# Optimization experiments

Measured on AMD Instinct MI355X. Metric: run time of the kernel, lower is better.

## Reference

```python
import jax, jax.numpy as jnp
import numpy as np
import math

D_K = 64
DROP_P = 0.5

def setup_inputs() -> dict:
    key = jax.random.key(0)
    kq, kk, kv, km = jax.random.split(key, 4)
    B, S, d = 32, 2048, D_K
    Q = jax.random.normal(kq, (B, S, d), dtype=jnp.float32)
    K = jax.random.normal(kk, (B, S, d), dtype=jnp.float32)
    V = jax.random.normal(kv, (B, S, d), dtype=jnp.float32)
    # Bernoulli(keep_prob) mask for training-mode dropout (p=0.5)
    dropout_mask = jax.random.bernoulli(km, 1.0 - DROP_P, (B, S, S))
    return {"Q": Q, "K": K, "V": V, "dropout_mask": dropout_mask}

def reference(Q, K, V, dropout_mask):
    # attn = softmax(Q K^T / sqrt(d_k)); dropout; y = attn V
    scale = 1.0 / math.sqrt(D_K)
    scores = jnp.einsum('bqd,bkd->bqk', Q, K) * scale   # [B,S,S]
    attn = jax.nn.softmax(scores, axis=-1)
    keep_scale = 1.0 / (1.0 - DROP_P)
    attn = jnp.where(dropout_mask, attn * keep_scale, 0.0)
    y = jnp.einsum('bqk,bkd->bqd', attn, V)             # [B,S,d]
    return (y, attn)
```

## Files before the change

### kernel.cpp

```cpp
#include <hip/hip_runtime.h>
#include <hip/hip_bf16.h>
#include <stdint.h>

#define SQ 2048
#define DK 64
#define NB 32
#define TQ 16
#define EW 2064
#define SCL 0.18033688011112042f

typedef __attribute__((ext_vector_type(8))) short short8;
typedef __attribute__((ext_vector_type(4))) float f32x4;
typedef __attribute__((ext_vector_type(4))) unsigned u32x4;
typedef __attribute__((ext_vector_type(2))) unsigned u32x2;

__device__ __forceinline__ unsigned f2bf_u(float x) {
    unsigned u = __builtin_bit_cast(unsigned, x);
    u += 0x7fffu + ((u >> 16) & 1u);
    return u >> 16;
}
__device__ __forceinline__ float bf2f(unsigned h) {
    return __builtin_bit_cast(float, h << 16);
}
__device__ __forceinline__ float bf2f_hi(unsigned u) {
    return __builtin_bit_cast(float, u & 0xffff0000u);
}
__device__ __forceinline__ unsigned cvtpk_bf16(float lo, float hi) {
    unsigned r;
    asm("v_cvt_pk_bf16_f32 %0, %1, %2" : "=v"(r) : "v"(lo), "v"(hi));
    return r;
}
__device__ __forceinline__ void split8(const float* p, short8& h, short8& l) {
    f32x4 a = *(const f32x4*)p;
    f32x4 b = *(const f32x4*)(p + 4);
    #pragma unroll
    for (int j = 0; j < 4; ++j) {
        unsigned ua = f2bf_u(a[j]);
        h[j] = (short)ua; l[j] = (short)f2bf_u(a[j] - bf2f(ua));
        unsigned ub = f2bf_u(b[j]);
        h[j + 4] = (short)ub; l[j + 4] = (short)f2bf_u(b[j] - bf2f(ub));
    }
}

__global__ __launch_bounds__(256) void prep_kernel(
    const float* __restrict__ K, const float* __restrict__ V,
    const unsigned* __restrict__ Mk,
    unsigned short* __restrict__ Khi, unsigned short* __restrict__ Klo,
    unsigned short* __restrict__ Vt, unsigned* __restrict__ Mkb)
{
    __shared__ float vtile[64][65];
    const int t = threadIdx.x;

    if (blockIdx.x >= NB * 32) {
        const size_t w = (size_t)(blockIdx.x - NB * 32) * 256 + t;
        const unsigned* p = Mk + w * 32;
        unsigned bits = 0;
        #pragma unroll
        for (int j = 0; j < 8; ++j) {
            const u32x4 v = *(const u32x4*)(p + j * 4);
            bits |= (v[0] ? 1u : 0u) << (j * 4 + 0);
            bits |= (v[1] ? 1u : 0u) << (j * 4 + 1);
            bits |= (v[2] ? 1u : 0u) << (j * 4 + 2);
            bits |= (v[3] ? 1u : 0u) << (j * 4 + 3);
        }
        Mkb[w] = bits;
        return;
    }

    const int b  = blockIdx.x >> 5;
    const int s0 = (blockIdx.x & 31) << 6;
    const size_t base = ((size_t)b * SQ + s0) * DK + (size_t)t * 16;

    {
        short8 h0, l0, h1, l1;
        split8(K + base,     h0, l0);
        split8(K + base + 8, h1, l1);
        *(short8*)(Khi + base)     = h0;
        *(short8*)(Khi + base + 8) = h1;
        *(short8*)(Klo + base)     = l0;
        *(short8*)(Klo + base + 8) = l1;
    }
    {
        const int sr = t >> 2, dc = (t & 3) << 4;
        #pragma unroll
        for (int u = 0; u < 16; u += 4) {
            f32x4 v = *(const f32x4*)(V + base + u);
            vtile[sr][dc + u + 0] = v[0];
            vtile[sr][dc + u + 1] = v[1];
            vtile[sr][dc + u + 2] = v[2];
            vtile[sr][dc + u + 3] = v[3];
        }
    }
    __syncthreads();
    #pragma unroll
    for (int rep = 0; rep < 16; ++rep) {
        const int idx = rep * 256 + t;
        const int d = idx >> 6, s = idx & 63;
        Vt[((size_t)b * DK + d) * SQ + s0 + s] = (unsigned short)f2bf_u(vtile[s][d]);
    }
}

__global__ __launch_bounds__(512, 4) void sdpa_main(
    const float* __restrict__ Q, const unsigned short* __restrict__ Khi,
    const unsigned short* __restrict__ Klo, const unsigned short* __restrict__ Vt,
    const unsigned* __restrict__ Mkb, float* __restrict__ Yout, float* __restrict__ Aout)
{
    __shared__ __align__(16) unsigned short e_lds[TQ][EW];
    __shared__ float yp[4][TQ][16];
    __shared__ float rsum[8][TQ];
    __shared__ float i2s[TQ];

    const int tid  = threadIdx.x;
    const int lane = tid & 63;
    const int wv   = tid >> 6;
    const int m16  = lane & 15;
    const int kq   = lane >> 4;
    const int koff = kq * 8;

    const int bx  = blockIdx.x;
    const int xcd = bx & 7;
    const int j   = bx >> 3;
    const int b   = xcd * 4 + (j >> 7);
    const int q0  = (j & 127) * TQ;

    short8 qh[2], ql[2];
    {
        const float* qrow = Q + ((size_t)b * SQ + q0 + m16) * DK;
        split8(qrow + koff,      qh[0], ql[0]);
        split8(qrow + 32 + koff, qh[1], ql[1]);
    }

    const unsigned* mrow = Mkb + ((size_t)b * SQ + q0 + m16) * (SQ / 32) + wv * 8;
    const u32x4 mA = *(const u32x4*)mrow;
    const u32x4 mB = *(const u32x4*)(mrow + 4);

    float rs = 0.f;
    {
        const size_t krow = ((size_t)b * SQ + wv * 256 + m16) * DK;
        const unsigned short* khp = Khi + krow;
        const unsigned short* klp = Klo + krow;
        const int xw = (m16 & 7) << 3;
        #pragma unroll
        for (int t = 0; t < 16; ++t) {
            const int off = t * 16 * DK;
            const short8 kh0 = *(const short8*)(khp + off + koff);
            const short8 kh1 = *(const short8*)(khp + off + 32 + koff);
            const short8 kl0 = *(const short8*)(klp + off + koff);
            const short8 kl1 = *(const short8*)(klp + off + 32 + koff);
            f32x4 a0 = {0.f, 0.f, 0.f, 0.f};
            f32x4 a1 = {0.f, 0.f, 0.f, 0.f};
            a0 = __builtin_amdgcn_mfma_f32_16x16x32_bf16(kh0, qh[0], a0, 0, 0, 0);
            a1 = __builtin_amdgcn_mfma_f32_16x16x32_bf16(kh1, qh[1], a1, 0, 0, 0);
            a0 = __builtin_amdgcn_mfma_f32_16x16x32_bf16(kh0, ql[0], a0, 0, 0, 0);
            a1 = __builtin_amdgcn_mfma_f32_16x16x32_bf16(kh1, ql[1], a1, 0, 0, 0);
            a0 = __builtin_amdgcn_mfma_f32_16x16x32_bf16(kl0, qh[0], a0, 0, 0, 0);
            a1 = __builtin_amdgcn_mfma_f32_16x16x32_bf16(kl1, qh[1], a1, 0, 0, 0);
            const float e0 = __builtin_amdgcn_exp2f((a0[0] + a1[0]) * SCL);
            const float e1 = __builtin_amdgcn_exp2f((a0[1] + a1[1]) * SCL);
            const float e2 = __builtin_amdgcn_exp2f((a0[2] + a1[2]) * SCL);
            const float e3 = __builtin_amdgcn_exp2f((a0[3] + a1[3]) * SCL);
            rs += (e0 + e1) + (e2 + e3);
            const unsigned mword = (t < 8) ? mA[t >> 1] : mB[(t >> 1) - 4];
            const unsigned bits = mword >> ((t & 1) * 16 + kq * 4);
            const float p0 = (bits & 1u) ? e0 : 0.f;
            const float p1 = (bits & 2u) ? e1 : 0.f;
            const float p2 = (bits & 4u) ? e2 : 0.f;
            const float p3 = (bits & 8u) ? e3 : 0.f;
            u32x2 pk;
            pk[0] = cvtpk_bf16(p0, p1);
            pk[1] = cvtpk_bf16(p2, p3);
            *(u32x2*)&e_lds[m16][(wv * 256 + t * 16 + kq * 4) ^ xw] = pk;
        }
    }
    rs += __shfl_xor(rs, 16);
    rs += __shfl_xor(rs, 32);
    if (lane < 16) rsum[wv][lane] = rs;
    __syncthreads();
    if (tid < 16) {
        float s = 0.f;
        #pragma unroll
        for (int w = 0; w < 8; ++w) s += rsum[w][tid];
        i2s[tid] = 2.0f / s;
    }
    __syncthreads();

    const int cr = tid >> 5;
    const int cc = (tid & 31) * 8;
    const int xc = (cr & 7) << 3;
    const float i2 = i2s[cr];
    const size_t crow = ((size_t)b * SQ + q0 + cr) * SQ + cc;

    const int g    = wv >> 1;
    const int par  = wv & 1;
    const int xm   = (m16 & 7) << 3;
    const unsigned short* vrow = Vt + ((size_t)b * DK + g * 16 + m16) * SQ;
    f32x4 acc = {0.f, 0.f, 0.f, 0.f};

    #define CSTRIPE(s)                                                            \
    {                                                                             \
        const u32x4 ev = *(const u32x4*)&e_lds[cr][((s) * 256 + cc) ^ xc];        \
        f32x4 o0, o1;                                                             \
        o0[0] = bf2f(ev[0] & 0xffffu) * i2;  o0[1] = bf2f_hi(ev[0]) * i2;         \
        o0[2] = bf2f(ev[1] & 0xffffu) * i2;  o0[3] = bf2f_hi(ev[1]) * i2;         \
        o1[0] = bf2f(ev[2] & 0xffffu) * i2;  o1[1] = bf2f_hi(ev[2]) * i2;         \
        o1[2] = bf2f(ev[3] & 0xffffu) * i2;  o1[3] = bf2f_hi(ev[3]) * i2;         \
        __builtin_nontemporal_store(o0, (f32x4*)(Aout + crow + (s) * 256));       \
        __builtin_nontemporal_store(o1, (f32x4*)(Aout + crow + (s) * 256 + 4));   \
    }
    #define PVCHUNK4(c0)                                                          \
    {                                                                             \
        _Pragma("unroll")                                                         \
        for (int c = (c0); c < (c0) + 4; ++c) {                                   \
            const int kl = par * 1024 + c * 32;                                   \
            const short8 af = *(const short8*)&e_lds[m16][(kl + koff) ^ xm];      \
            const short8 vf = *(const short8*)(vrow + kl + koff);                 \
            acc = __builtin_amdgcn_mfma_f32_16x16x32_bf16(af, vf, acc, 0, 0, 0);  \
        }                                                                         \
    }

    CSTRIPE(0) PVCHUNK4(0)
    CSTRIPE(1) PVCHUNK4(4)
    CSTRIPE(2) PVCHUNK4(8)
    CSTRIPE(3) PVCHUNK4(12)
    CSTRIPE(4) PVCHUNK4(16)
    CSTRIPE(5) PVCHUNK4(20)
    CSTRIPE(6) PVCHUNK4(24)
    CSTRIPE(7) PVCHUNK4(28)

    #undef PVCHUNK4
    #undef CSTRIPE

    if (par == 1) {
        #pragma unroll
        for (int r = 0; r < 4; ++r) yp[g][kq * 4 + r][m16] = acc[r];
    }
    __syncthreads();
    if (par == 0) {
        #pragma unroll
        for (int r = 0; r < 4; ++r) {
            const float yv = (acc[r] + yp[g][kq * 4 + r][m16]) * i2s[kq * 4 + r];
            Yout[((size_t)b * SQ + q0 + kq * 4 + r) * DK + g * 16 + m16] = yv;
        }
    }
}

extern "C" void kernel_launch(void* const* d_in, const int* in_sizes, int n_in,
                              void* d_out, int out_size, void* d_ws, size_t ws_size,
                              hipStream_t stream) {
    const float*    Q  = (const float*)d_in[0];
    const float*    K  = (const float*)d_in[1];
    const float*    V  = (const float*)d_in[2];
    const unsigned* Mk = (const unsigned*)d_in[3];
    float* Yout = (float*)d_out;
    float* Aout = (float*)d_out + (size_t)NB * SQ * DK;

    const size_t NEL = (size_t)NB * SQ * DK;
    unsigned short* Khi = (unsigned short*)d_ws;
    unsigned short* Klo = Khi + NEL;
    unsigned short* Vt  = Klo + NEL;
    unsigned*       Mkb = (unsigned*)(Vt + NEL);

    const int NPREP = NB * 32;
    const int NMKP  = (int)((size_t)NB * SQ * (SQ / 32) / 256);
    prep_kernel<<<dim3(NPREP + NMKP), dim3(256), 0, stream>>>(K, V, Mk, Khi, Klo, Vt, Mkb);
    sdpa_main<<<dim3(NB * (SQ / TQ)), dim3(512), 0, stream>>>(
        Q, Khi, Klo, Vt, Mkb, Yout, Aout);
}
```

Baseline: 530.7 us.

## Split key dimension across two blocks with redundant row-sum and partial-Y reduction

Each query tile is now handled by two blocks, each owning half of the key range. Every block still computes the full QK^T row sums so normalisation stays exact, but only the owning waves write bf16 probabilities to shared memory. Each block then does half of the attention output stores and half of the PV product, writing partial Y to a workspace that a new kernel sums. Shared memory per block is halved and launch bounds are raised to allow more resident blocks. The cost is doubled QK^T matmul and exp work, an extra kernel launch, and extra global traffic for partial Y.

```diff
diff --git a/kernel.cpp b/kernel.cpp
--- a/kernel.cpp
+++ b/kernel.cpp
@@ -6,7 +6,8 @@
 #define DK 64
 #define NB 32
 #define TQ 16
-#define EW 2064
+#define KH 1024
+#define EW 1032
 #define SCL 0.18033688011112042f
 
 typedef __attribute__((ext_vector_type(8))) short short8;
@@ -100,12 +101,12 @@
     }
 }
 
-__global__ __launch_bounds__(512, 4) void sdpa_main(
+__global__ __launch_bounds__(512, 8) void sdpa_main(
     const float* __restrict__ Q, const unsigned short* __restrict__ Khi,
     const unsigned short* __restrict__ Klo, const unsigned short* __restrict__ Vt,
-    const unsigned* __restrict__ Mkb, float* __restrict__ Yout, float* __restrict__ Aout)
+    const unsigned* __restrict__ Mkb, float* __restrict__ Yp, float* __restrict__ Aout)
 {
-    __shared__ __align__(16) unsigned short e_lds[TQ][EW];
+    __shared__ __align__(16) unsigned short e_half[TQ][EW];
     __shared__ float yp[4][TQ][16];
     __shared__ float rsum[8][TQ];
     __shared__ float i2s[TQ];
@@ -117,11 +118,16 @@
     const int kq   = lane >> 4;
     const int koff = kq * 8;
 
-    const int bx  = blockIdx.x;
-    const int xcd = bx & 7;
-    const int j   = bx >> 3;
-    const int b   = xcd * 4 + (j >> 7);
-    const int q0  = (j & 127) * TQ;
+    const int bx   = blockIdx.x;
+    const int xcd  = bx & 7;
+    const int j    = bx >> 3;
+    const int b    = xcd * 4 + (j >> 8);
+    const int rest = j & 255;
+    const int q0   = (rest >> 1) * TQ;
+    const int kh   = rest & 1;
+
+    const int wlocal = wv & 3;
+    const bool owned = (wv >> 2) == kh;
 
     short8 qh[2], ql[2];
     {
@@ -129,10 +135,6 @@
         split8(qrow + koff,      qh[0], ql[0]);
         split8(qrow + 32 + koff, qh[1], ql[1]);
     }
-
-    const unsigned* mrow = Mkb + ((size_t)b * SQ + q0 + m16) * (SQ / 32) + wv * 8;
-    const u32x4 mA = *(const u32x4*)mrow;
-    const u32x4 mB = *(const u32x4*)(mrow + 4);
 
     float rs = 0.f;
     {
@@ -140,36 +142,63 @@
         const unsigned short* khp = Khi + krow;
         const unsigned short* klp = Klo + krow;
         const int xw = (m16 & 7) << 3;
-        #pragma unroll
-        for (int t = 0; t < 16; ++t) {
-            const int off = t * 16 * DK;
-            const short8 kh0 = *(const short8*)(khp + off + koff);
-            const short8 kh1 = *(const short8*)(khp + off + 32 + koff);
-            const short8 kl0 = *(const short8*)(klp + off + koff);
-            const short8 kl1 = *(const short8*)(klp + off + 32 + koff);
-            f32x4 a0 = {0.f, 0.f, 0.f, 0.f};
-            f32x4 a1 = {0.f, 0.f, 0.f, 0.f};
-            a0 = __builtin_amdgcn_mfma_f32_16x16x32_bf16(kh0, qh[0], a0, 0, 0, 0);
-            a1 = __builtin_amdgcn_mfma_f32_16x16x32_bf16(kh1, qh[1], a1, 0, 0, 0);
-            a0 = __builtin_amdgcn_mfma_f32_16x16x32_bf16(kh0, ql[0], a0, 0, 0, 0);
-            a1 = __builtin_amdgcn_mfma_f32_16x16x32_bf16(kh1, ql[1], a1, 0, 0, 0);
-            a0 = __builtin_amdgcn_mfma_f32_16x16x32_bf16(kl0, qh[0], a0, 0, 0, 0);
-            a1 = __builtin_amdgcn_mfma_f32_16x16x32_bf16(kl1, qh[1], a1, 0, 0, 0);
-            const float e0 = __builtin_amdgcn_exp2f((a0[0] + a1[0]) * SCL);
-            const float e1 = __builtin_amdgcn_exp2f((a0[1] + a1[1]) * SCL);
-            const float e2 = __builtin_amdgcn_exp2f((a0[2] + a1[2]) * SCL);
-            const float e3 = __builtin_amdgcn_exp2f((a0[3] + a1[3]) * SCL);
-            rs += (e0 + e1) + (e2 + e3);
-            const unsigned mword = (t < 8) ? mA[t >> 1] : mB[(t >> 1) - 4];
-            const unsigned bits = mword >> ((t & 1) * 16 + kq * 4);
-            const float p0 = (bits & 1u) ? e0 : 0.f;
-            const float p1 = (bits & 2u) ? e1 : 0.f;
-            const float p2 = (bits & 4u) ? e2 : 0.f;
-            const float p3 = (bits & 8u) ? e3 : 0.f;
-            u32x2 pk;
-            pk[0] = cvtpk_bf16(p0, p1);
-            pk[1] = cvtpk_bf16(p2, p3);
-            *(u32x2*)&e_lds[m16][(wv * 256 + t * 16 + kq * 4) ^ xw] = pk;
+
+        if (owned) {
+            const unsigned* mrow = Mkb + ((size_t)b * SQ + q0 + m16) * (SQ / 32) + wv * 8;
+            const u32x4 mA = *(const u32x4*)mrow;
+            const u32x4 mB = *(const u32x4*)(mrow + 4);
+            #pragma unroll
+            for (int t = 0; t < 16; ++t) {
+                const int off = t * 16 * DK;
+                const short8 kh0 = *(const short8*)(khp + off + koff);
+                const short8 kh1 = *(const short8*)(khp + off + 32 + koff);
+                const short8 kl0 = *(const short8*)(klp + off + koff);
+                const short8 kl1 = *(const short8*)(klp + off + 32 + koff);
+                f32x4 a0 = {0.f, 0.f, 0.f, 0.f};
+                f32x4 a1 = {0.f, 0.f, 0.f, 0.f};
+                a0 = __builtin_amdgcn_mfma_f32_16x16x32_bf16(kh0, qh[0], a0, 0, 0, 0);
+                a1 = __builtin_amdgcn_mfma_f32_16x16x32_bf16(kh1, qh[1], a1, 0, 0, 0);
+                a0 = __builtin_amdgcn_mfma_f32_16x16x32_bf16(kh0, ql[0], a0, 0, 0, 0);
+                a1 = __builtin_amdgcn_mfma_f32_16x16x32_bf16(kh1, ql[1], a1, 0, 0, 0);
+                a0 = __builtin_amdgcn_mfma_f32_16x16x32_bf16(kl0, qh[0], a0, 0, 0, 0);
+                a1 = __builtin_amdgcn_mfma_f32_16x16x32_bf16(kl1, qh[1], a1, 0, 0, 0);
+                const float e0 = __builtin_amdgcn_exp2f((a0[0] + a1[0]) * SCL);
+                const float e1 = __builtin_amdgcn_exp2f((a0[1] + a1[1]) * SCL);
+                const float e2 = __builtin_amdgcn_exp2f((a0[2] + a1[2]) * SCL);
+                const float e3 = __builtin_amdgcn_exp2f((a0[3] + a1[3]) * SCL);
+                rs += (e0 + e1) + (e2 + e3);
+                const unsigned mword = (t < 8) ? mA[t >> 1] : mB[(t >> 1) - 4];
+                const unsigned bits = mword >> ((t & 1) * 16 + kq * 4);
+                const float p0 = (bits & 1u) ? e0 : 0.f;
+                const float p1 = (bits & 2u) ? e1 : 0.f;
+                const float p2 = (bits & 4u) ? e2 : 0.f;
+                const float p3 = (bits & 8u) ? e3 : 0.f;
+                u32x2 pk;
+                pk[0] = cvtpk_bf16(p0, p1);
+                pk[1] = cvtpk_bf16(p2, p3);
+                *(u32x2*)&e_half[m16][(wlocal * 256 + t * 16 + kq * 4) ^ xw] = pk;
+            }
+        } else {
+            #pragma unroll
+            for (int t = 0; t < 16; ++t) {
+                const int off = t * 16 * DK;
+                const short8 kh0 = *(const short8*)(khp + off + koff);
+                const short8 kh1 = *(const short8*)(khp + off + 32 + koff);
+                const short8 kl0 = *(const short8*)(klp + off + koff);
+                const short8 kl1 = *(const short8*)(klp + off + 32 + koff);
+                f32x4 a0 = {0.f, 0.f, 0.f, 0.f};
+                f32x4 a1 = {0.f, 0.f, 0.f, 0.f};
+                a0 = __builtin_amdgcn_mfma_f32_16x16x32_bf16(kh0, qh[0], a0, 0, 0, 0);
+                a1 = __builtin_amdgcn_mfma_f32_16x16x32_bf16(kh1, qh[1], a1, 0, 0, 0);
+                a0 = __builtin_amdgcn_mfma_f32_16x16x32_bf16(kh0, ql[0], a0, 0, 0, 0);
+                a1 = __builtin_amdgcn_mfma_f32_16x16x32_bf16(kh1, ql[1], a1, 0, 0, 0);
+                a0 = __builtin_amdgcn_mfma_f32_16x16x32_bf16(kl0, qh[0], a0, 0, 0, 0);
+                a1 = __builtin_amdgcn_mfma_f32_16x16x32_bf16(kl1, qh[1], a1, 0, 0, 0);
+                rs += (__builtin_amdgcn_exp2f((a0[0] + a1[0]) * SCL)
+                     + __builtin_amdgcn_exp2f((a0[1] + a1[1]) * SCL))
+                    + (__builtin_amdgcn_exp2f((a0[2] + a1[2]) * SCL)
+                     + __builtin_amdgcn_exp2f((a0[3] + a1[3]) * SCL));
+            }
         }
     }
     rs += __shfl_xor(rs, 16);
@@ -188,17 +217,17 @@
     const int cc = (tid & 31) * 8;
     const int xc = (cr & 7) << 3;
     const float i2 = i2s[cr];
-    const size_t crow = ((size_t)b * SQ + q0 + cr) * SQ + cc;
-
-    const int g    = wv >> 1;
-    const int par  = wv & 1;
-    const int xm   = (m16 & 7) << 3;
-    const unsigned short* vrow = Vt + ((size_t)b * DK + g * 16 + m16) * SQ;
+    const size_t crow = ((size_t)b * SQ + q0 + cr) * SQ + (size_t)kh * KH + cc;
+
+    const int g   = wv >> 1;
+    const int par = wv & 1;
+    const int xm  = (m16 & 7) << 3;
+    const unsigned short* vrow = Vt + ((size_t)b * DK + g * 16 + m16) * SQ + (size_t)kh * KH;
     f32x4 acc = {0.f, 0.f, 0.f, 0.f};
 
     #define CSTRIPE(s)                                                            \
     {                                                                             \
-        const u32x4 ev = *(const u32x4*)&e_lds[cr][((s) * 256 + cc) ^ xc];        \
+        const u32x4 ev = *(const u32x4*)&e_half[cr][((s) * 256 + cc) ^ xc];       \
         f32x4 o0, o1;                                                             \
         o0[0] = bf2f(ev[0] & 0xffffu) * i2;  o0[1] = bf2f_hi(ev[0]) * i2;         \
         o0[2] = bf2f(ev[1] & 0xffffu) * i2;  o0[3] = bf2f_hi(ev[1]) * i2;         \
@@ -211,8 +240,8 @@
     {                                                                             \
         _Pragma("unroll")                                                         \
         for (int c = (c0); c < (c0) + 4; ++c) {                                   \
-            const int kl = par * 1024 + c * 32;                                   \
-            const short8 af = *(const short8*)&e_lds[m16][(kl + koff) ^ xm];      \
+            const int kl = par * 512 + c * 32;                                    \
+            const short8 af = *(const short8*)&e_half[m16][(kl + koff) ^ xm];     \
             const short8 vf = *(const short8*)(vrow + kl + koff);                 \
             acc = __builtin_amdgcn_mfma_f32_16x16x32_bf16(af, vf, acc, 0, 0, 0);  \
         }                                                                         \
@@ -222,10 +251,6 @@
     CSTRIPE(1) PVCHUNK4(4)
     CSTRIPE(2) PVCHUNK4(8)
     CSTRIPE(3) PVCHUNK4(12)
-    CSTRIPE(4) PVCHUNK4(16)
-    CSTRIPE(5) PVCHUNK4(20)
-    CSTRIPE(6) PVCHUNK4(24)
-    CSTRIPE(7) PVCHUNK4(28)
 
     #undef PVCHUNK4
     #undef CSTRIPE
@@ -238,10 +263,23 @@
     if (par == 0) {
         #pragma unroll
         for (int r = 0; r < 4; ++r) {
-            const float yv = (acc[r] + yp[g][kq * 4 + r][m16]) * i2s[kq * 4 + r];
-            Yout[((size_t)b * SQ + q0 + kq * 4 + r) * DK + g * 16 + m16] = yv;
+            const int row = kq * 4 + r;
+            const float yv = (acc[r] + yp[g][row][m16]) * i2s[row];
+            __builtin_nontemporal_store(yv,
+                Yp + ((size_t)(kh * NB + b) * SQ + q0 + row) * DK + g * 16 + m16);
         }
     }
+}
+
+__global__ __launch_bounds__(256) void yred_kernel(
+    const float* __restrict__ Yp, float* __restrict__ Yout)
+{
+    const size_t NEL = (size_t)NB * SQ * DK;
+    const size_t i = ((size_t)blockIdx.x * 256 + threadIdx.x) * 4;
+    f32x4 a = *(const f32x4*)(Yp + i);
+    f32x4 b = *(const f32x4*)(Yp + NEL + i);
+    f32x4 s = a + b;
+    __builtin_nontemporal_store(s, (f32x4*)(Yout + i));
 }
 
 extern "C" void kernel_launch(void* const* d_in, const int* in_sizes, int n_in,
@@ -259,10 +297,12 @@
     unsigned short* Klo = Khi + NEL;
     unsigned short* Vt  = Klo + NEL;
     unsigned*       Mkb = (unsigned*)(Vt + NEL);
+    float*          Yp  = (float*)(Mkb + NEL / 2);
 
     const int NPREP = NB * 32;
     const int NMKP  = (int)((size_t)NB * SQ * (SQ / 32) / 256);
     prep_kernel<<<dim3(NPREP + NMKP), dim3(256), 0, stream>>>(K, V, Mk, Khi, Klo, Vt, Mkb);
-    sdpa_main<<<dim3(NB * (SQ / TQ)), dim3(512), 0, stream>>>(
-        Q, Khi, Klo, Vt, Mkb, Yout, Aout);
-}
+    sdpa_main<<<dim3(NB * (SQ / TQ) * 2), dim3(512), 0, stream>>>(
+        Q, Khi, Klo, Vt, Mkb, Yp, Aout);
+    yred_kernel<<<dim3((unsigned)(NEL / 1024)), dim3(256), 0, stream>>>(Yp, Yout);
+}
```

Result: slower. 854.1 us (+60.9%).
